# Kernel tuning notes

Hardware: AMD Instinct MI355X
Metric: run time of the kernel (lower is better)

The kernel has to match this reference:

```python
import jax, jax.numpy as jnp
import numpy as np

EMBED_DIM = 256
NUM_HEADS = 8
WINDOW = 64
HEAD_DIM = EMBED_DIM // NUM_HEADS


def setup_inputs() -> dict:
    key = jax.random.key(0)
    k_x, k_w, k_ow = jax.random.split(key, 3)
    B, S, E = 2, 4096, EMBED_DIM
    x = jax.random.normal(k_x, (B, S, E), dtype=jnp.float32)
    # nn.MultiheadAttention params: packed in_proj (q,k,v) and out_proj
    bound = 1.0 / np.sqrt(E)
    in_proj_w = jax.random.uniform(k_w, (3 * E, E), jnp.float32, -bound, bound)
    in_proj_b = jnp.zeros((3 * E,), jnp.float32)
    out_w = jax.random.uniform(k_ow, (E, E), jnp.float32, -bound, bound)
    out_b = jnp.zeros((E,), jnp.float32)
    return {"x": x, "in_proj_w": in_proj_w, "in_proj_b": in_proj_b,
            "out_w": out_w, "out_b": out_b}


def reference(x, in_proj_w, in_proj_b, out_w, out_b):
    B, S, E = x.shape
    H, D = NUM_HEADS, HEAD_DIM
    # packed qkv projection (torch Linear: y = x @ W^T + b)
    qkv = jnp.einsum('bse,fe->bsf', x, in_proj_w) + in_proj_b  # [B,S,3E]
    q, k, v = jnp.split(qkv, 3, axis=-1)
    q = q.reshape(B, S, H, D).transpose(0, 2, 1, 3)  # [B,H,S,D]
    k = k.reshape(B, S, H, D).transpose(0, 2, 1, 3)
    v = v.reshape(B, S, H, D).transpose(0, 2, 1, 3)
    scale = 1.0 / jnp.sqrt(jnp.asarray(D, x.dtype))
    scores = jnp.einsum('bhqd,bhkd->bhqk', q * scale, k)  # [B,H,S,S]
    idx = jnp.arange(S)
    band = jnp.abs(idx[:, None] - idx[None, :]) <= WINDOW  # [S,S]
    neg = jnp.asarray(-1e9, scores.dtype)
    scores = jnp.where(band[None, None, :, :], scores, neg)
    attn = jax.nn.softmax(scores, axis=-1)
    out = jnp.einsum('bhqk,bhkd->bhqd', attn, v)  # [B,H,S,D]
    out = out.transpose(0, 2, 1, 3).reshape(B, S, E)
    return jnp.einsum('bse,fe->bsf', out, out_w) + out_b
```

## Files before the change

kernel.cpp:

```cpp
#include <hip/hip_runtime.h>
#include <hip/hip_bf16.h>

#define S_LEN 4096
#define EMB   256
#define NHEAD 8
#define HDIM  32
#define WIN   64
#define BATCH 2

typedef __attribute__((ext_vector_type(8))) short short8;
typedef __attribute__((ext_vector_type(4))) float floatx4;

static __device__ __forceinline__ unsigned int bf16_rn(float x) {
    unsigned int u = __float_as_uint(x);
    return (u + 0x7FFFu + ((u >> 16) & 1u)) >> 16;
}
static __device__ __forceinline__ void split2(float x, unsigned int& hi, unsigned int& lo) {
    hi = bf16_rn(x);
    const float hf = __uint_as_float(hi << 16);
    lo = bf16_rn(x - hf);
}
static __device__ __forceinline__ void split_store4(unsigned short* hp, unsigned short* lp, float4 v) {
    unsigned int h0, l0, h1, l1, h2, l2, h3, l3;
    split2(v.x, h0, l0); split2(v.y, h1, l1);
    split2(v.z, h2, l2); split2(v.w, h3, l3);
    uint2 hv, lv;
    hv.x = h0 | (h1 << 16); hv.y = h2 | (h3 << 16);
    lv.x = l0 | (l1 << 16); lv.y = l2 | (l3 << 16);
    *(uint2*)hp = hv;
    *(uint2*)lp = lv;
}

#define LDA 40

__global__ __launch_bounds__(256) void qkv_proj_kernel(
    const float* __restrict__ X, const float* __restrict__ W,
    const float* __restrict__ bias,
    float* __restrict__ Qb, float* __restrict__ Kb, float* __restrict__ Vb)
{
    __shared__ __align__(16) unsigned short Ah[128 * LDA], Al[128 * LDA];
    __shared__ __align__(16) unsigned short Bh[64 * LDA],  Bl[64 * LDA];
    const int tid = threadIdx.x;
    const int m0 = blockIdx.y * 128, n0 = blockIdx.x * 64;
    const int r0 = tid >> 3, c4 = tid & 7;
    const int lane = tid & 63, wv = tid >> 6;
    const int wm = (wv >> 1) * 64, wn = (wv & 1) * 32;
    const int lm = lane & 15, kq = lane >> 4;

    float4 ar[4], wr[2];
#pragma unroll
    for (int r = 0; r < 4; ++r)
        ar[r] = *(const float4*)(X + (size_t)(m0 + r0 + r * 32) * EMB + c4 * 4);
#pragma unroll
    for (int r = 0; r < 2; ++r)
        wr[r] = *(const float4*)(W + (size_t)(n0 + r0 + r * 32) * EMB + c4 * 4);

    floatx4 acc[4][2] = {};
    for (int t = 0; t < 8; ++t) {
        __syncthreads();
#pragma unroll
        for (int r = 0; r < 4; ++r)
            split_store4(&Ah[(r0 + r * 32) * LDA + c4 * 4], &Al[(r0 + r * 32) * LDA + c4 * 4], ar[r]);
#pragma unroll
        for (int r = 0; r < 2; ++r)
            split_store4(&Bh[(r0 + r * 32) * LDA + c4 * 4], &Bl[(r0 + r * 32) * LDA + c4 * 4], wr[r]);
        __syncthreads();
        if (t < 7) {
            const int k0 = (t + 1) * 32;
#pragma unroll
            for (int r = 0; r < 4; ++r)
                ar[r] = *(const float4*)(X + (size_t)(m0 + r0 + r * 32) * EMB + k0 + c4 * 4);
#pragma unroll
            for (int r = 0; r < 2; ++r)
                wr[r] = *(const float4*)(W + (size_t)(n0 + r0 + r * 32) * EMB + k0 + c4 * 4);
        }
        short8 a_h[4], a_l[4], b_h[2], b_l[2];
#pragma unroll
        for (int mt = 0; mt < 4; ++mt) {
            a_h[mt] = *(const short8*)&Ah[(wm + mt * 16 + lm) * LDA + kq * 8];
            a_l[mt] = *(const short8*)&Al[(wm + mt * 16 + lm) * LDA + kq * 8];
        }
#pragma unroll
        for (int nt = 0; nt < 2; ++nt) {
            b_h[nt] = *(const short8*)&Bh[(wn + nt * 16 + lm) * LDA + kq * 8];
            b_l[nt] = *(const short8*)&Bl[(wn + nt * 16 + lm) * LDA + kq * 8];
        }
#pragma unroll
        for (int mt = 0; mt < 4; ++mt)
#pragma unroll
            for (int nt = 0; nt < 2; ++nt) {
                acc[mt][nt] = __builtin_amdgcn_mfma_f32_16x16x32_bf16(a_h[mt], b_h[nt], acc[mt][nt], 0, 0, 0);
                acc[mt][nt] = __builtin_amdgcn_mfma_f32_16x16x32_bf16(a_h[mt], b_l[nt], acc[mt][nt], 0, 0, 0);
                acc[mt][nt] = __builtin_amdgcn_mfma_f32_16x16x32_bf16(a_l[mt], b_h[nt], acc[mt][nt], 0, 0, 0);
            }
    }
#pragma unroll
    for (int nt = 0; nt < 2; ++nt) {
        const int f = n0 + wn + nt * 16 + lm;
        const int which = f >> 8;
        const int h = (f & 255) >> 5, d = f & 31;
        float* dst = (which == 0) ? Qb : ((which == 1) ? Kb : Vb);
        const float sc = (which == 0) ? 0.17677669529663687f : 1.0f;
        const float bf = bias[f];
#pragma unroll
        for (int mt = 0; mt < 4; ++mt)
#pragma unroll
            for (int r = 0; r < 4; ++r) {
                const int m = m0 + wm + mt * 16 + kq * 4 + r;
                const int b = m >> 12, s = m & (S_LEN - 1);
                dst[(((size_t)b * NHEAD + h) * S_LEN + s) * HDIM + d] = (acc[mt][nt][r] + bf) * sc;
            }
    }
}

__global__ __launch_bounds__(256) void out_proj_kernel(
    const float* __restrict__ A, const float* __restrict__ W,
    const float* __restrict__ bias, float* __restrict__ C)
{
    __shared__ __align__(16) unsigned short Ah[128 * LDA], Al[128 * LDA];
    __shared__ __align__(16) unsigned short Bh[64 * LDA],  Bl[64 * LDA];
    const int tid = threadIdx.x;
    const int m0 = blockIdx.y * 128, n0 = blockIdx.x * 64;
    const int r0 = tid >> 3, c4 = tid & 7;
    const int lane = tid & 63, wv = tid >> 6;
    const int wm = (wv >> 1) * 64, wn = (wv & 1) * 32;
    const int lm = lane & 15, kq = lane >> 4;

    float4 ar[4], wr[2];
#pragma unroll
    for (int r = 0; r < 4; ++r)
        ar[r] = *(const float4*)(A + (size_t)(m0 + r0 + r * 32) * EMB + c4 * 4);
#pragma unroll
    for (int r = 0; r < 2; ++r)
        wr[r] = *(const float4*)(W + (size_t)(n0 + r0 + r * 32) * EMB + c4 * 4);

    floatx4 acc[4][2] = {};
    for (int t = 0; t < 8; ++t) {
        __syncthreads();
#pragma unroll
        for (int r = 0; r < 4; ++r)
            split_store4(&Ah[(r0 + r * 32) * LDA + c4 * 4], &Al[(r0 + r * 32) * LDA + c4 * 4], ar[r]);
#pragma unroll
        for (int r = 0; r < 2; ++r)
            split_store4(&Bh[(r0 + r * 32) * LDA + c4 * 4], &Bl[(r0 + r * 32) * LDA + c4 * 4], wr[r]);
        __syncthreads();
        if (t < 7) {
            const int k0 = (t + 1) * 32;
#pragma unroll
            for (int r = 0; r < 4; ++r)
                ar[r] = *(const float4*)(A + (size_t)(m0 + r0 + r * 32) * EMB + k0 + c4 * 4);
#pragma unroll
            for (int r = 0; r < 2; ++r)
                wr[r] = *(const float4*)(W + (size_t)(n0 + r0 + r * 32) * EMB + k0 + c4 * 4);
        }
        short8 a_h[4], a_l[4], b_h[2], b_l[2];
#pragma unroll
        for (int mt = 0; mt < 4; ++mt) {
            a_h[mt] = *(const short8*)&Ah[(wm + mt * 16 + lm) * LDA + kq * 8];
            a_l[mt] = *(const short8*)&Al[(wm + mt * 16 + lm) * LDA + kq * 8];
        }
#pragma unroll
        for (int nt = 0; nt < 2; ++nt) {
            b_h[nt] = *(const short8*)&Bh[(wn + nt * 16 + lm) * LDA + kq * 8];
            b_l[nt] = *(const short8*)&Bl[(wn + nt * 16 + lm) * LDA + kq * 8];
        }
#pragma unroll
        for (int mt = 0; mt < 4; ++mt)
#pragma unroll
            for (int nt = 0; nt < 2; ++nt) {
                acc[mt][nt] = __builtin_amdgcn_mfma_f32_16x16x32_bf16(a_h[mt], b_h[nt], acc[mt][nt], 0, 0, 0);
                acc[mt][nt] = __builtin_amdgcn_mfma_f32_16x16x32_bf16(a_h[mt], b_l[nt], acc[mt][nt], 0, 0, 0);
                acc[mt][nt] = __builtin_amdgcn_mfma_f32_16x16x32_bf16(a_l[mt], b_h[nt], acc[mt][nt], 0, 0, 0);
            }
    }
#pragma unroll
    for (int nt = 0; nt < 2; ++nt) {
        const int f = n0 + wn + nt * 16 + lm;
        const float bf = bias[f];
#pragma unroll
        for (int mt = 0; mt < 4; ++mt)
#pragma unroll
            for (int r = 0; r < 4; ++r) {
                const int m = m0 + wm + mt * 16 + kq * 4 + r;
                C[(size_t)m * EMB + f] = acc[mt][nt][r] + bf;
            }
    }
}

#define KT_STRIDE 204
#define PS_STRIDE 196
#define VS_STRIDE 36
#define QT_STRIDE 68

__global__ __launch_bounds__(256) void local_attn_kernel(
    const float* __restrict__ Qb, const float* __restrict__ Kb,
    const float* __restrict__ Vb, float* __restrict__ Ab)
{
    __shared__ __align__(16) float SA[192 * VS_STRIDE];
    __shared__ __align__(16) float SB[64 * PS_STRIDE];
    __shared__ float Lrs[64];
    const int tid = threadIdx.x;
    const int q0 = blockIdx.x * 64;
    const int h = blockIdx.y, b = blockIdx.z;
    const int jmin = max(0, q0 - WIN);
    const int jmax = min(S_LEN - 1, q0 + 63 + WIN);
    const int nk = jmax - jmin + 1;
    const size_t bhS = ((size_t)b * NHEAD + h) * S_LEN;
    const float* Qg = Qb + (bhS + q0) * HDIM;
    const float* Kg = Kb + (bhS + jmin) * HDIM;
    const float* Vg = Vb + (bhS + jmin) * HDIM;

    float* Qt = SA;
    float* Vs = SA;
    float* Kt = SB;
    float* Ps = SB;

    const int r0 = tid >> 3, c4 = tid & 7;
#pragma unroll
    for (int r = 0; r < 2; ++r) {
        const int row = r0 + r * 32;
        const float4 v = *(const float4*)&Qg[row * HDIM + c4 * 4];
        Qt[(c4 * 4 + 0) * QT_STRIDE + row] = v.x;
        Qt[(c4 * 4 + 1) * QT_STRIDE + row] = v.y;
        Qt[(c4 * 4 + 2) * QT_STRIDE + row] = v.z;
        Qt[(c4 * 4 + 3) * QT_STRIDE + row] = v.w;
    }
#pragma unroll
    for (int r = 0; r < 6; ++r) {
        const int t = r0 + r * 32;
        const int tc = min(t, nk - 1);
        const float4 v = *(const float4*)&Kg[tc * HDIM + c4 * 4];
        Kt[(c4 * 4 + 0) * KT_STRIDE + t] = v.x;
        Kt[(c4 * 4 + 1) * KT_STRIDE + t] = v.y;
        Kt[(c4 * 4 + 2) * KT_STRIDE + t] = v.z;
        Kt[(c4 * 4 + 3) * KT_STRIDE + t] = v.w;
    }
    __syncthreads();

    const int tx = tid & 15, ty = tid >> 4;
    float s[4][12] = {};
#pragma unroll 4
    for (int kk = 0; kk < 32; ++kk) {
        const float4 qf = *(const float4*)&Qt[kk * QT_STRIDE + ty * 4];
        const float4 k0f = *(const float4*)&Kt[kk * KT_STRIDE + tx * 12];
        const float4 k1f = *(const float4*)&Kt[kk * KT_STRIDE + tx * 12 + 4];
        const float4 k2f = *(const float4*)&Kt[kk * KT_STRIDE + tx * 12 + 8];
        const float qm[4] = {qf.x, qf.y, qf.z, qf.w};
        const float kn[12] = {k0f.x, k0f.y, k0f.z, k0f.w,
                              k1f.x, k1f.y, k1f.z, k1f.w,
                              k2f.x, k2f.y, k2f.z, k2f.w};
#pragma unroll
        for (int qi = 0; qi < 4; ++qi)
#pragma unroll
            for (int jj = 0; jj < 12; ++jj)
                s[qi][jj] = fmaf(qm[qi], kn[jj], s[qi][jj]);
    }
    float l[4];
#pragma unroll
    for (int qi = 0; qi < 4; ++qi) {
        const int q = q0 + ty * 4 + qi;
        float m = -1e30f;
#pragma unroll
        for (int jj = 0; jj < 12; ++jj) {
            const int j = jmin + tx * 12 + jj;
            const bool valid = (j >= q - WIN) && (j <= q + WIN) && (j <= jmax);
            const float sv = valid ? s[qi][jj] : -1e30f;
            s[qi][jj] = sv;
            m = fmaxf(m, sv);
        }
        m = fmaxf(m, __shfl_xor(m, 1));
        m = fmaxf(m, __shfl_xor(m, 2));
        m = fmaxf(m, __shfl_xor(m, 4));
        m = fmaxf(m, __shfl_xor(m, 8));
        float ls = 0.f;
#pragma unroll
        for (int jj = 0; jj < 12; ++jj) {
            const float e = __expf(s[qi][jj] - m);
            s[qi][jj] = e;
            ls += e;
        }
        ls += __shfl_xor(ls, 1);
        ls += __shfl_xor(ls, 2);
        ls += __shfl_xor(ls, 4);
        ls += __shfl_xor(ls, 8);
        l[qi] = ls;
    }
    __syncthreads();

#pragma unroll
    for (int qi = 0; qi < 4; ++qi) {
        float* pr = &Ps[(ty * 4 + qi) * PS_STRIDE + tx * 12];
        float4 w0, w1, w2;
        w0.x = s[qi][0]; w0.y = s[qi][1]; w0.z = s[qi][2]; w0.w = s[qi][3];
        w1.x = s[qi][4]; w1.y = s[qi][5]; w1.z = s[qi][6]; w1.w = s[qi][7];
        w2.x = s[qi][8]; w2.y = s[qi][9]; w2.z = s[qi][10]; w2.w = s[qi][11];
        *(float4*)(pr + 0) = w0;
        *(float4*)(pr + 4) = w1;
        *(float4*)(pr + 8) = w2;
    }
    if (tx == 0) {
#pragma unroll
        for (int qi = 0; qi < 4; ++qi) Lrs[ty * 4 + qi] = 1.f / l[qi];
    }
#pragma unroll
    for (int r = 0; r < 6; ++r) {
        const int t = r0 + r * 32;
        const int tc = min(t, nk - 1);
        const float4 v = *(const float4*)&Vg[tc * HDIM + c4 * 4];
        *(float4*)&Vs[t * VS_STRIDE + c4 * 4] = v;
    }
    __syncthreads();

    const int q = tid & 63, dg = tid >> 6;
    const float rl = Lrs[q];
    float o[8] = {};
    const float* prow = &Ps[q * PS_STRIDE];
#pragma unroll 4
    for (int kc = 0; kc < 48; ++kc) {
        const float4 p4 = *(const float4*)(prow + kc * 4);
        const float pf[4] = {p4.x, p4.y, p4.z, p4.w};
#pragma unroll
        for (int jj = 0; jj < 4; ++jj) {
            const int k = kc * 4 + jj;
            const float4 v0 = *(const float4*)&Vs[k * VS_STRIDE + dg * 8];
            const float4 v1 = *(const float4*)&Vs[k * VS_STRIDE + dg * 8 + 4];
            o[0] = fmaf(pf[jj], v0.x, o[0]);
            o[1] = fmaf(pf[jj], v0.y, o[1]);
            o[2] = fmaf(pf[jj], v0.z, o[2]);
            o[3] = fmaf(pf[jj], v0.w, o[3]);
            o[4] = fmaf(pf[jj], v1.x, o[4]);
            o[5] = fmaf(pf[jj], v1.y, o[5]);
            o[6] = fmaf(pf[jj], v1.z, o[6]);
            o[7] = fmaf(pf[jj], v1.w, o[7]);
        }
    }
    float* og = Ab + ((size_t)b * S_LEN + q0 + q) * EMB + h * HDIM + dg * 8;
    float4 w0, w1;
    w0.x = o[0] * rl; w0.y = o[1] * rl; w0.z = o[2] * rl; w0.w = o[3] * rl;
    w1.x = o[4] * rl; w1.y = o[5] * rl; w1.z = o[6] * rl; w1.w = o[7] * rl;
    *(float4*)og = w0;
    *(float4*)(og + 4) = w1;
}

extern "C" void kernel_launch(void* const* d_in, const int* in_sizes, int n_in,
                              void* d_out, int out_size, void* d_ws, size_t ws_size,
                              hipStream_t stream) {
    const float* x  = (const float*)d_in[0];
    const float* wi = (const float*)d_in[1];
    const float* bi = (const float*)d_in[2];
    const float* wo = (const float*)d_in[3];
    const float* bo = (const float*)d_in[4];
    float* out = (float*)d_out;

    const size_t per = (size_t)BATCH * NHEAD * S_LEN * HDIM;
    float* Qb = (float*)d_ws;
    float* Kb = Qb + per;
    float* Vb = Kb + per;
    float* Ab = Vb + per;

    qkv_proj_kernel<<<dim3(768 / 64, 8192 / 128), 256, 0, stream>>>(x, wi, bi, Qb, Kb, Vb);
    local_attn_kernel<<<dim3(S_LEN / 64, NHEAD, BATCH), 256, 0, stream>>>(Qb, Kb, Vb, Ab);
    out_proj_kernel<<<dim3(256 / 64, 8192 / 128), 256, 0, stream>>>(Ab, wo, bo, out);
}
```

Measured before the change: 131.6 us.

## Move local attention QK and PV products onto bf16 MFMA with split precision

Rewrites the local attention kernel so Q·K^T runs on bf16 MFMA instructions, using a hi/lo split of Q and K to keep near-fp32 accuracy. P·V runs on single-bf16 MFMA. The scalar FMA outer-product loops are replaced by per-wave 16-row tiles, with the softmax done in registers on the MFMA accumulator layout. Each wave writes its P tile to shared memory as bf16 and V is stored transposed as bf16. This cuts ALU work and shared-memory traffic, at the cost of bf16 rounding of P and V, conversion overhead, and scattered 16-bit transposed stores to shared memory.

```diff
diff --git a/kernel.cpp b/kernel.cpp
--- a/kernel.cpp
+++ b/kernel.cpp
@@ -187,18 +187,19 @@
     }
 }
 
-#define KT_STRIDE 204
-#define PS_STRIDE 196
-#define VS_STRIDE 36
-#define QT_STRIDE 68
+#define AKS 40
+#define AVS 200
+#define APS 200
 
 __global__ __launch_bounds__(256) void local_attn_kernel(
     const float* __restrict__ Qb, const float* __restrict__ Kb,
     const float* __restrict__ Vb, float* __restrict__ Ab)
 {
-    __shared__ __align__(16) float SA[192 * VS_STRIDE];
-    __shared__ __align__(16) float SB[64 * PS_STRIDE];
-    __shared__ float Lrs[64];
+    __shared__ __align__(16) unsigned short Qh[64 * AKS], Ql[64 * AKS];
+    __shared__ __align__(16) unsigned short Kh[192 * AKS], Kl[192 * AKS];
+    __shared__ __align__(16) unsigned short Vt[32 * AVS];
+    __shared__ __align__(16) unsigned short Pw[4 * 16 * APS];
+
     const int tid = threadIdx.x;
     const int q0 = blockIdx.x * 64;
     const int h = blockIdx.y, b = blockIdx.z;
@@ -210,136 +211,109 @@
     const float* Kg = Kb + (bhS + jmin) * HDIM;
     const float* Vg = Vb + (bhS + jmin) * HDIM;
 
-    float* Qt = SA;
-    float* Vs = SA;
-    float* Kt = SB;
-    float* Ps = SB;
-
     const int r0 = tid >> 3, c4 = tid & 7;
 #pragma unroll
     for (int r = 0; r < 2; ++r) {
         const int row = r0 + r * 32;
         const float4 v = *(const float4*)&Qg[row * HDIM + c4 * 4];
-        Qt[(c4 * 4 + 0) * QT_STRIDE + row] = v.x;
-        Qt[(c4 * 4 + 1) * QT_STRIDE + row] = v.y;
-        Qt[(c4 * 4 + 2) * QT_STRIDE + row] = v.z;
-        Qt[(c4 * 4 + 3) * QT_STRIDE + row] = v.w;
+        split_store4(&Qh[row * AKS + c4 * 4], &Ql[row * AKS + c4 * 4], v);
     }
 #pragma unroll
     for (int r = 0; r < 6; ++r) {
         const int t = r0 + r * 32;
         const int tc = min(t, nk - 1);
         const float4 v = *(const float4*)&Kg[tc * HDIM + c4 * 4];
-        Kt[(c4 * 4 + 0) * KT_STRIDE + t] = v.x;
-        Kt[(c4 * 4 + 1) * KT_STRIDE + t] = v.y;
-        Kt[(c4 * 4 + 2) * KT_STRIDE + t] = v.z;
-        Kt[(c4 * 4 + 3) * KT_STRIDE + t] = v.w;
-    }
-    __syncthreads();
-
-    const int tx = tid & 15, ty = tid >> 4;
-    float s[4][12] = {};
-#pragma unroll 4
-    for (int kk = 0; kk < 32; ++kk) {
-        const float4 qf = *(const float4*)&Qt[kk * QT_STRIDE + ty * 4];
-        const float4 k0f = *(const float4*)&Kt[kk * KT_STRIDE + tx * 12];
-        const float4 k1f = *(const float4*)&Kt[kk * KT_STRIDE + tx * 12 + 4];
-        const float4 k2f = *(const float4*)&Kt[kk * KT_STRIDE + tx * 12 + 8];
-        const float qm[4] = {qf.x, qf.y, qf.z, qf.w};
-        const float kn[12] = {k0f.x, k0f.y, k0f.z, k0f.w,
-                              k1f.x, k1f.y, k1f.z, k1f.w,
-                              k2f.x, k2f.y, k2f.z, k2f.w};
-#pragma unroll
-        for (int qi = 0; qi < 4; ++qi)
-#pragma unroll
-            for (int jj = 0; jj < 12; ++jj)
-                s[qi][jj] = fmaf(qm[qi], kn[jj], s[qi][jj]);
-    }
-    float l[4];
-#pragma unroll
-    for (int qi = 0; qi < 4; ++qi) {
-        const int q = q0 + ty * 4 + qi;
-        float m = -1e30f;
-#pragma unroll
-        for (int jj = 0; jj < 12; ++jj) {
-            const int j = jmin + tx * 12 + jj;
-            const bool valid = (j >= q - WIN) && (j <= q + WIN) && (j <= jmax);
-            const float sv = valid ? s[qi][jj] : -1e30f;
-            s[qi][jj] = sv;
-            m = fmaxf(m, sv);
-        }
-        m = fmaxf(m, __shfl_xor(m, 1));
-        m = fmaxf(m, __shfl_xor(m, 2));
-        m = fmaxf(m, __shfl_xor(m, 4));
-        m = fmaxf(m, __shfl_xor(m, 8));
-        float ls = 0.f;
-#pragma unroll
-        for (int jj = 0; jj < 12; ++jj) {
-            const float e = __expf(s[qi][jj] - m);
-            s[qi][jj] = e;
-            ls += e;
-        }
-        ls += __shfl_xor(ls, 1);
-        ls += __shfl_xor(ls, 2);
-        ls += __shfl_xor(ls, 4);
-        ls += __shfl_xor(ls, 8);
-        l[qi] = ls;
-    }
-    __syncthreads();
-
-#pragma unroll
-    for (int qi = 0; qi < 4; ++qi) {
-        float* pr = &Ps[(ty * 4 + qi) * PS_STRIDE + tx * 12];
-        float4 w0, w1, w2;
-        w0.x = s[qi][0]; w0.y = s[qi][1]; w0.z = s[qi][2]; w0.w = s[qi][3];
-        w1.x = s[qi][4]; w1.y = s[qi][5]; w1.z = s[qi][6]; w1.w = s[qi][7];
-        w2.x = s[qi][8]; w2.y = s[qi][9]; w2.z = s[qi][10]; w2.w = s[qi][11];
-        *(float4*)(pr + 0) = w0;
-        *(float4*)(pr + 4) = w1;
-        *(float4*)(pr + 8) = w2;
-    }
-    if (tx == 0) {
-#pragma unroll
-        for (int qi = 0; qi < 4; ++qi) Lrs[ty * 4 + qi] = 1.f / l[qi];
+        split_store4(&Kh[t * AKS + c4 * 4], &Kl[t * AKS + c4 * 4], v);
     }
 #pragma unroll
     for (int r = 0; r < 6; ++r) {
         const int t = r0 + r * 32;
         const int tc = min(t, nk - 1);
         const float4 v = *(const float4*)&Vg[tc * HDIM + c4 * 4];
-        *(float4*)&Vs[t * VS_STRIDE + c4 * 4] = v;
+        Vt[(c4 * 4 + 0) * AVS + t] = (unsigned short)bf16_rn(v.x);
+        Vt[(c4 * 4 + 1) * AVS + t] = (unsigned short)bf16_rn(v.y);
+        Vt[(c4 * 4 + 2) * AVS + t] = (unsigned short)bf16_rn(v.z);
+        Vt[(c4 * 4 + 3) * AVS + t] = (unsigned short)bf16_rn(v.w);
     }
     __syncthreads();
 
-    const int q = tid & 63, dg = tid >> 6;
-    const float rl = Lrs[q];
-    float o[8] = {};
-    const float* prow = &Ps[q * PS_STRIDE];
-#pragma unroll 4
-    for (int kc = 0; kc < 48; ++kc) {
-        const float4 p4 = *(const float4*)(prow + kc * 4);
-        const float pf[4] = {p4.x, p4.y, p4.z, p4.w};
-#pragma unroll
-        for (int jj = 0; jj < 4; ++jj) {
-            const int k = kc * 4 + jj;
-            const float4 v0 = *(const float4*)&Vs[k * VS_STRIDE + dg * 8];
-            const float4 v1 = *(const float4*)&Vs[k * VS_STRIDE + dg * 8 + 4];
-            o[0] = fmaf(pf[jj], v0.x, o[0]);
-            o[1] = fmaf(pf[jj], v0.y, o[1]);
-            o[2] = fmaf(pf[jj], v0.z, o[2]);
-            o[3] = fmaf(pf[jj], v0.w, o[3]);
-            o[4] = fmaf(pf[jj], v1.x, o[4]);
-            o[5] = fmaf(pf[jj], v1.y, o[5]);
-            o[6] = fmaf(pf[jj], v1.z, o[6]);
-            o[7] = fmaf(pf[jj], v1.w, o[7]);
-        }
-    }
-    float* og = Ab + ((size_t)b * S_LEN + q0 + q) * EMB + h * HDIM + dg * 8;
-    float4 w0, w1;
-    w0.x = o[0] * rl; w0.y = o[1] * rl; w0.z = o[2] * rl; w0.w = o[3] * rl;
-    w1.x = o[4] * rl; w1.y = o[5] * rl; w1.z = o[6] * rl; w1.w = o[7] * rl;
-    *(float4*)og = w0;
-    *(float4*)(og + 4) = w1;
+    const int lane = tid & 63, wv = tid >> 6;
+    const int lm = lane & 15, quad = lane >> 4;
+    const int qbase = wv * 16;
+
+    const short8 qh = *(const short8*)&Qh[(qbase + lm) * AKS + quad * 8];
+    const short8 ql = *(const short8*)&Ql[(qbase + lm) * AKS + quad * 8];
+
+    floatx4 sacc[12];
+#pragma unroll
+    for (int nt = 0; nt < 12; ++nt) {
+        const short8 bh = *(const short8*)&Kh[(nt * 16 + lm) * AKS + quad * 8];
+        const short8 bl = *(const short8*)&Kl[(nt * 16 + lm) * AKS + quad * 8];
+        floatx4 a = {};
+        a = __builtin_amdgcn_mfma_f32_16x16x32_bf16(qh, bh, a, 0, 0, 0);
+        a = __builtin_amdgcn_mfma_f32_16x16x32_bf16(qh, bl, a, 0, 0, 0);
+        a = __builtin_amdgcn_mfma_f32_16x16x32_bf16(ql, bh, a, 0, 0, 0);
+        sacc[nt] = a;
+    }
+
+    const int qg = q0 + qbase + quad * 4;
+    float mx[4] = {-1e30f, -1e30f, -1e30f, -1e30f};
+#pragma unroll
+    for (int nt = 0; nt < 12; ++nt) {
+        const int slot = nt * 16 + lm;
+        const int keyg = jmin + slot;
+#pragma unroll
+        for (int r = 0; r < 4; ++r) {
+            const int qr = qg + r;
+            const bool valid = (slot < nk) && (keyg >= qr - WIN) && (keyg <= qr + WIN);
+            const float sv = valid ? sacc[nt][r] : -1e30f;
+            sacc[nt][r] = sv;
+            mx[r] = fmaxf(mx[r], sv);
+        }
+    }
+#pragma unroll
+    for (int r = 0; r < 4; ++r) {
+        mx[r] = fmaxf(mx[r], __shfl_xor(mx[r], 1));
+        mx[r] = fmaxf(mx[r], __shfl_xor(mx[r], 2));
+        mx[r] = fmaxf(mx[r], __shfl_xor(mx[r], 4));
+        mx[r] = fmaxf(mx[r], __shfl_xor(mx[r], 8));
+    }
+    float l[4] = {0.f, 0.f, 0.f, 0.f};
+    unsigned short* Pme = &Pw[wv * 16 * APS];
+#pragma unroll
+    for (int nt = 0; nt < 12; ++nt)
+#pragma unroll
+        for (int r = 0; r < 4; ++r) {
+            const float p = __expf(sacc[nt][r] - mx[r]);
+            l[r] += p;
+            Pme[(quad * 4 + r) * APS + nt * 16 + lm] = (unsigned short)bf16_rn(p);
+        }
+#pragma unroll
+    for (int r = 0; r < 4; ++r) {
+        l[r] += __shfl_xor(l[r], 1);
+        l[r] += __shfl_xor(l[r], 2);
+        l[r] += __shfl_xor(l[r], 4);
+        l[r] += __shfl_xor(l[r], 8);
+    }
+    const float rl[4] = {1.f / l[0], 1.f / l[1], 1.f / l[2], 1.f / l[3]};
+
+    floatx4 oacc[2] = {};
+#pragma unroll
+    for (int ks = 0; ks < 6; ++ks) {
+        const short8 ap  = *(const short8*)&Pme[lm * APS + ks * 32 + quad * 8];
+        const short8 bv0 = *(const short8*)&Vt[lm * AVS + ks * 32 + quad * 8];
+        const short8 bv1 = *(const short8*)&Vt[(16 + lm) * AVS + ks * 32 + quad * 8];
+        oacc[0] = __builtin_amdgcn_mfma_f32_16x16x32_bf16(ap, bv0, oacc[0], 0, 0, 0);
+        oacc[1] = __builtin_amdgcn_mfma_f32_16x16x32_bf16(ap, bv1, oacc[1], 0, 0, 0);
+    }
+#pragma unroll
+    for (int nt = 0; nt < 2; ++nt)
+#pragma unroll
+        for (int r = 0; r < 4; ++r) {
+            const int qrow = qbase + quad * 4 + r;
+            Ab[((size_t)b * S_LEN + q0 + qrow) * EMB + h * HDIM + nt * 16 + lm]
+                = oacc[nt][r] * rl[r];
+        }
 }
 
 extern "C" void kernel_launch(void* const* d_in, const int* in_sizes, int n_in,
```

Measured after the change: 117.0 us. -11.1%, faster.
